# Kernel tuning notes

Measured on AMD Instinct MI355X. Metric: run time of the kernel, lower is better.

Reference implementation:

```python
import jax, jax.numpy as jnp
import numpy as np
import math

B, T, D = 2, 2048, 512      # batch, n_tp, input_dim
DM, H = 64, 16              # per-head d_model, nhead


def setup_inputs() -> dict:
    key = jax.random.key(0)
    ks = jax.random.split(key, 12)
    s = 0.02
    return {
        "data": jax.random.normal(ks[0], (B, T, D), jnp.float32),
        "mask": jax.random.uniform(ks[1], (B, T, D), jnp.float32),
        "wq": jax.random.normal(ks[2], (D, DM * H), jnp.float32) * s,
        "bq": jnp.zeros((DM * H,), jnp.float32),
        "wk": jax.random.normal(ks[3], (D, DM * H), jnp.float32) * s,
        "bk": jnp.zeros((DM * H,), jnp.float32),
        "wv": jax.random.normal(ks[4], (D, DM * H), jnp.float32) * s,
        "bv": jnp.zeros((DM * H,), jnp.float32),
        "wo": jax.random.normal(ks[5], (DM * H, D), jnp.float32) * s,
        "bo": jnp.zeros((D,), jnp.float32),
    }


def reference(data, mask, wq, bq, wk, bk, wv, bv, wo, bo):
    b, t, d = data.shape
    # NOTE: torch code splits proj as (d_model, nhead): head index is fastest-varying
    def split_heads(x):  # [b,t,DM*H] -> [b,H,t,DM]
        return x.reshape(b, t, DM, H).transpose(0, 3, 1, 2)

    q = split_heads(data @ wq + bq)
    k = split_heads(data @ wk + bk)
    v = split_heads(data @ wv + bv)

    scores = jnp.einsum("bhqd,bhkd->bhqk", q, k) / math.sqrt(DM)
    # padded key positions: rows of mask that sum to exactly 0
    pad = (jnp.sum(mask, axis=-1) == 0.0)  # [b, t] (key axis)
    scores = jnp.where(pad[:, None, None, :], -1e9, scores)
    attn = jax.nn.softmax(scores, axis=-1)  # dropout = identity (eval mode)
    out = jnp.einsum("bhqk,bhkd->bhqd", attn, v)
    # merge as (nhead, d_model) — matches torch permute(0,2,1,3).reshape
    out = out.transpose(0, 2, 1, 3).reshape(b, t, H * DM)
    return out @ wo + bo
```

## Files before the change

kernel.cpp:

```cpp
#include <hip/hip_runtime.h>
#include <hip/hip_bf16.h>

#define B_  2
#define T_  2048
#define D_  512
#define DM_ 64
#define H_  16
#define NQ_ (DM_*H_)

typedef __bf16 bf16x8 __attribute__((ext_vector_type(8)));
typedef __bf16 bf16x4 __attribute__((ext_vector_type(4)));
typedef float  f32x4  __attribute__((ext_vector_type(4)));
typedef unsigned int u32;

static __device__ __forceinline__ __bf16 bfc(float x) { return (__bf16)x; }
static __device__ __forceinline__ unsigned short f2bf(float x) {
    __bf16 b = (__bf16)x;
    unsigned short u;
    __builtin_memcpy(&u, &b, 2);
    return u;
}

#if __has_builtin(__builtin_amdgcn_exp2f)
static __device__ __forceinline__ float EXP2(float x) { return __builtin_amdgcn_exp2f(x); }
#else
static __device__ __forceinline__ float EXP2(float x) {
    float r; asm("v_exp_f32 %0, %1\ns_nop 0" : "=v"(r) : "v"(x)); return r;
}
#endif

#define GLOAD16(gp, lp) \
    __builtin_amdgcn_global_load_lds((const __attribute__((address_space(1))) u32*)(gp), \
                                     (__attribute__((address_space(3))) u32*)(lp), 16, 0, 0)

__global__ __launch_bounds__(256)
void prep_kernel(const float* __restrict__ mask, float* __restrict__ padb,
                 const float* __restrict__ data, unsigned short* __restrict__ dataB,
                 const float* __restrict__ wq, const float* __restrict__ wk,
                 const float* __restrict__ wv, unsigned short* __restrict__ btall,
                 const float* __restrict__ wo, unsigned short* __restrict__ wot)
{
    __shared__ float t[32][33];
    const int bid = blockIdx.x;
    const int tid = threadIdx.x;
    if (bid < 1024) {
        const int row  = bid * 4 + (tid >> 6);
        const int lane = tid & 63;
        const float* p = mask + (size_t)row * D_;
        float4 a = *(const float4*)&p[lane * 8];
        float4 b = *(const float4*)&p[lane * 8 + 4];
        float s = a.x + a.y + a.z + a.w + b.x + b.y + b.z + b.w;
#pragma unroll
        for (int off = 32; off; off >>= 1) s += __shfl_down(s, off);
        if (lane == 0) padb[row] = (s == 0.0f) ? -1e9f : 0.0f;
    } else if (bid < 2048) {
        int i = ((bid - 1024) * 256 + tid) * 8;
        float4 a = *(const float4*)&data[i];
        float4 b = *(const float4*)&data[i + 4];
        bf16x8 u = {bfc(a.x), bfc(a.y), bfc(a.z), bfc(a.w),
                    bfc(b.x), bfc(b.y), bfc(b.z), bfc(b.w)};
        *(bf16x8*)&dataB[i] = u;
    } else if (bid < 3584) {
        const int idx = bid - 2048;
        const int z = idx >> 9, rem = idx & 511;
        const int c0 = (rem & 31) * 32, r0 = (rem >> 5) * 32;
        const float* in = (z == 0) ? wq : (z == 1) ? wk : wv;
        unsigned short* out = btall + (size_t)z * NQ_ * D_;
        const int tx = tid & 31, ty = tid >> 5;
#pragma unroll
        for (int i = 0; i < 4; ++i)
            t[ty * 4 + i][tx] = in[(size_t)(r0 + ty * 4 + i) * NQ_ + c0 + tx];
        __syncthreads();
#pragma unroll
        for (int i = 0; i < 4; ++i)
            out[(size_t)(c0 + ty * 4 + i) * D_ + r0 + tx] = f2bf(t[tx][ty * 4 + i]);
    } else {
        const int idx = bid - 3584;
        const int c0 = (idx & 15) * 32, r0 = (idx >> 4) * 32;
        const int tx = tid & 31, ty = tid >> 5;
#pragma unroll
        for (int i = 0; i < 4; ++i)
            t[ty * 4 + i][tx] = wo[(size_t)(r0 + ty * 4 + i) * D_ + c0 + tx];
        __syncthreads();
#pragma unroll
        for (int i = 0; i < 4; ++i)
            wot[(size_t)(c0 + ty * 4 + i) * NQ_ + r0 + tx] = f2bf(t[tx][ty * 4 + i]);
    }
}

__global__ __launch_bounds__(256)
void mgemm_qkv_kernel(const unsigned short* __restrict__ A,
                      const unsigned short* __restrict__ BtAll,
                      const float* __restrict__ bq, const float* __restrict__ bk,
                      const float* __restrict__ bv,
                      unsigned short* __restrict__ Qh, unsigned short* __restrict__ Kh,
                      unsigned short* __restrict__ Vt, float alpha_q)
{
    const int K = D_;
    __shared__ __align__(16) unsigned short Al[2][128 * 64];
    __shared__ __align__(16) unsigned short Bl[2][128 * 64];

    const int tid = threadIdx.x;
    const int w  = tid >> 6, l = tid & 63;
    const int lo = l & 15,  g = l >> 4;
    const int wri = w >> 1, wci = w & 1;
    const int m0 = blockIdx.y * 128, n0 = blockIdx.x * 128;
    const int lrow = l >> 3;
    const int lslot = (l & 7) ^ lrow;

    f32x4 acc[4][4] = {};
    const int nk = K >> 6;

#pragma unroll
    for (int p = 0; p < 4; ++p) {
        int br = w * 32 + p * 8;
        GLOAD16(A     + (size_t)(m0 + br + lrow) * K + lslot * 8, (char*)Al[0] + br * 128);
        GLOAD16(BtAll + (size_t)(n0 + br + lrow) * K + lslot * 8, (char*)Bl[0] + br * 128);
    }
    __syncthreads();

    for (int t = 0; t < nk; ++t) {
        const int cur = t & 1;
        if (t + 1 < nk) {
            const int k0 = (t + 1) << 6;
#pragma unroll
            for (int p = 0; p < 4; ++p) {
                int br = w * 32 + p * 8;
                GLOAD16(A     + (size_t)(m0 + br + lrow) * K + k0 + lslot * 8,
                        (char*)Al[cur ^ 1] + br * 128);
                GLOAD16(BtAll + (size_t)(n0 + br + lrow) * K + k0 + lslot * 8,
                        (char*)Bl[cur ^ 1] + br * 128);
            }
        }
#pragma unroll
        for (int kk = 0; kk < 2; ++kk) {
            bf16x8 af[4], bfr[4];
#pragma unroll
            for (int i = 0; i < 4; ++i) {
                int row = wri * 64 + i * 16 + lo;
                af[i] = *(const bf16x8*)&Al[cur][row * 64 + ((((kk << 2) + g) ^ (row & 7)) << 3)];
                int col = wci * 64 + i * 16 + lo;
                bfr[i] = *(const bf16x8*)&Bl[cur][col * 64 + ((((kk << 2) + g) ^ (col & 7)) << 3)];
            }
#pragma unroll
            for (int i = 0; i < 4; ++i)
#pragma unroll
                for (int j = 0; j < 4; ++j)
                    acc[i][j] = __builtin_amdgcn_mfma_f32_16x16x32_bf16(af[i], bfr[j], acc[i][j], 0, 0, 0);
        }
        __syncthreads();
    }

    const int seg = n0 >> 10;
    const int n0l = n0 & 1023;
    const float* bias = (seg == 0) ? bq : (seg == 1) ? bk : bv;
    const float alpha = (seg == 0) ? alpha_q : 1.0f;
    unsigned short* o16 = (seg == 0) ? Qh : (seg == 1) ? Kh : Vt;

    const int mb = m0 + wri * 64 + g * 4;
    float bb[4];
#pragma unroll
    for (int j = 0; j < 4; ++j) bb[j] = bias[n0l + wci * 64 + j * 16 + lo];
    const int head = lo;
    const int dmb  = (n0l >> 4) + wci * 4;
    if (seg < 2) {
#pragma unroll
        for (int i = 0; i < 4; ++i)
#pragma unroll
            for (int jj = 0; jj < 4; ++jj) {
                int m = mb + i * 16 + jj;
                int t = m & (T_ - 1), bidx = m >> 11;
                bf16x4 u = {bfc((acc[i][0][jj] + bb[0]) * alpha),
                            bfc((acc[i][1][jj] + bb[1]) * alpha),
                            bfc((acc[i][2][jj] + bb[2]) * alpha),
                            bfc((acc[i][3][jj] + bb[3]) * alpha)};
                *(bf16x4*)&o16[(((size_t)(bidx * H_ + head)) * T_ + t) * DM_ + dmb] = u;
            }
    } else {
#pragma unroll
        for (int i = 0; i < 4; ++i)
#pragma unroll
            for (int j = 0; j < 4; ++j) {
                int m = mb + i * 16;
                int t = m & (T_ - 1), bidx = m >> 11;
                bf16x4 u = {bfc(acc[i][j][0] + bb[j]), bfc(acc[i][j][1] + bb[j]),
                            bfc(acc[i][j][2] + bb[j]), bfc(acc[i][j][3] + bb[j])};
                *(bf16x4*)&o16[((size_t)(bidx * H_ + head) * DM_ + dmb + j) * T_ + t] = u;
            }
    }
}

__global__ __launch_bounds__(256)
void mgemm_out_kernel(const unsigned short* __restrict__ A,
                      const unsigned short* __restrict__ Bt,
                      const float* __restrict__ bias, float* __restrict__ out,
                      int M, int N, int K)
{
    __shared__ __align__(16) unsigned short Al[2][64 * 64];
    __shared__ __align__(16) unsigned short Bl[2][128 * 64];

    const int tid = threadIdx.x;
    const int w  = tid >> 6, l = tid & 63;
    const int lo = l & 15,  g = l >> 4;
    const int wri = w >> 1, wci = w & 1;
    const int m0 = blockIdx.y * 64, n0 = blockIdx.x * 128;
    const int lrow = l >> 3;
    const int lslot = (l & 7) ^ lrow;

    f32x4 acc[2][4] = {};
    const int nk = K >> 6;

#pragma unroll
    for (int p = 0; p < 2; ++p) {
        int br = w * 16 + p * 8;
        GLOAD16(A + (size_t)(m0 + br + lrow) * K + lslot * 8, (char*)Al[0] + br * 128);
    }
#pragma unroll
    for (int p = 0; p < 4; ++p) {
        int br = w * 32 + p * 8;
        GLOAD16(Bt + (size_t)(n0 + br + lrow) * K + lslot * 8, (char*)Bl[0] + br * 128);
    }
    __syncthreads();

    for (int t = 0; t < nk; ++t) {
        const int cur = t & 1;
        if (t + 1 < nk) {
            const int k0 = (t + 1) << 6;
#pragma unroll
            for (int p = 0; p < 2; ++p) {
                int br = w * 16 + p * 8;
                GLOAD16(A + (size_t)(m0 + br + lrow) * K + k0 + lslot * 8,
                        (char*)Al[cur ^ 1] + br * 128);
            }
#pragma unroll
            for (int p = 0; p < 4; ++p) {
                int br = w * 32 + p * 8;
                GLOAD16(Bt + (size_t)(n0 + br + lrow) * K + k0 + lslot * 8,
                        (char*)Bl[cur ^ 1] + br * 128);
            }
        }
#pragma unroll
        for (int kk = 0; kk < 2; ++kk) {
            bf16x8 af[2], bfr[4];
#pragma unroll
            for (int i = 0; i < 2; ++i) {
                int row = wri * 32 + i * 16 + lo;
                af[i] = *(const bf16x8*)&Al[cur][row * 64 + ((((kk << 2) + g) ^ (row & 7)) << 3)];
            }
#pragma unroll
            for (int j = 0; j < 4; ++j) {
                int col = wci * 64 + j * 16 + lo;
                bfr[j] = *(const bf16x8*)&Bl[cur][col * 64 + ((((kk << 2) + g) ^ (col & 7)) << 3)];
            }
#pragma unroll
            for (int i = 0; i < 2; ++i)
#pragma unroll
                for (int j = 0; j < 4; ++j)
                    acc[i][j] = __builtin_amdgcn_mfma_f32_16x16x32_bf16(af[i], bfr[j], acc[i][j], 0, 0, 0);
        }
        __syncthreads();
    }

    const int mb = m0 + wri * 32 + g * 4;
#pragma unroll
    for (int j = 0; j < 4; ++j) {
        int n = n0 + wci * 64 + j * 16 + lo;
        float bb = bias[n];
#pragma unroll
        for (int i = 0; i < 2; ++i)
#pragma unroll
            for (int jj = 0; jj < 4; ++jj) {
                int m = mb + i * 16 + jj;
                out[(size_t)m * N + n] = acc[i][j][jj] + bb;
            }
    }
}

__global__ __launch_bounds__(512, 4)
void attn_kernel(const unsigned short* __restrict__ Qh,
                 const unsigned short* __restrict__ Kh,
                 const unsigned short* __restrict__ Vt,
                 const float* __restrict__ padb,
                 unsigned short* __restrict__ ctx)
{
    __shared__ __align__(16) unsigned short Ks[2][64 * 64];
    __shared__ __align__(16) unsigned short Vs[2][64 * 64];
    __shared__ __align__(16) unsigned short Ps[8][16 * 64];

    const int tid  = threadIdx.x;
    const int w    = tid >> 6;
    const int l    = tid & 63;
    const int lo16 = l & 15;
    const int g    = l >> 4;
    const int lrow = l >> 3;
    const int lslot = (l & 7) ^ lrow;

    const int f   = blockIdx.x;
    const int s   = f >> 3;
    const int bh  = (f & 7) * 4 + (s >> 4);
    const int q0  = (s & 15) * 128;
    const int bb  = bh >> 4;
    const int hh  = bh & 15;

    bf16x8 qf[2];
    {
        const unsigned short* Qp =
            Qh + ((size_t)bh * T_ + q0 + w * 16 + lo16) * DM_ + g * 8;
        qf[0] = *(const bf16x8*)(Qp);
        qf[1] = *(const bf16x8*)(Qp + 32);
    }

    const unsigned short* Kg0 = Kh + (size_t)bh * T_ * DM_;
    const unsigned short* Vg0 = Vt + (size_t)bh * DM_ * T_;
    const float* pbase = padb + bb * T_;

    GLOAD16(Kg0 + (size_t)(w * 8 + lrow) * DM_ + lslot * 8, (char*)Ks[0] + w * 1024);
    GLOAD16(Vg0 + (size_t)(w * 8 + lrow) * T_ + lslot * 8, (char*)Vs[0] + w * 1024);
    __syncthreads();

    f32x4 oa[4] = {};
    f32x4 ls4 = {};
    char* Pb = (char*)&Ps[w][0];
    const int rswz = (lo16 & 7) << 4;

    for (int it = 0; it < T_ / 64; ++it) {
        const int cur = it & 1;
        const char* Kc = (const char*)Ks[cur];
        const char* Vc = (const char*)Vs[cur];
        if (it + 1 < T_ / 64) {
            const int ktn = (it + 1) * 64;
            GLOAD16(Kg0 + (size_t)(ktn + w * 8 + lrow) * DM_ + lslot * 8,
                    (char*)Ks[cur ^ 1] + w * 1024);
            GLOAD16(Vg0 + (size_t)(w * 8 + lrow) * T_ + ktn + lslot * 8,
                    (char*)Vs[cur ^ 1] + w * 1024);
        }

        f32x4 sa[4];
#pragma unroll
        for (int nt = 0; nt < 4; ++nt)
            sa[nt] = *(const f32x4*)&pbase[it * 64 + nt * 16 + g * 4];
        __builtin_amdgcn_s_setprio(1);
#pragma unroll
        for (int ks = 0; ks < 2; ++ks) {
#pragma unroll
            for (int nt = 0; nt < 4; ++nt) {
                int row = nt * 16 + lo16;
                int off = (row * 128 + ks * 64 + g * 16) ^ ((row & 7) << 4);
                bf16x8 kf = *(const bf16x8*)(Kc + off);
                sa[nt] = __builtin_amdgcn_mfma_f32_16x16x32_bf16(kf, qf[ks], sa[nt], 0, 0, 0);
            }
        }
        __builtin_amdgcn_s_setprio(0);

#pragma unroll
        for (int nt = 0; nt < 4; ++nt) {
            float e0 = EXP2(sa[nt][0]);
            float e1 = EXP2(sa[nt][1]);
            float e2 = EXP2(sa[nt][2]);
            float e3 = EXP2(sa[nt][3]);
            ls4 += (f32x4){e0, e1, e2, e3};
            bf16x4 pv4 = {bfc(e0), bfc(e1), bfc(e2), bfc(e3)};
            int wb = (lo16 * 128 + nt * 32 + g * 8) ^ rswz;
            *(bf16x4*)(Pb + wb) = pv4;
        }

        __builtin_amdgcn_s_setprio(1);
#pragma unroll
        for (int ks = 0; ks < 2; ++ks) {
            int poff = (lo16 * 128 + ks * 64 + g * 16) ^ rswz;
            bf16x8 pf = *(const bf16x8*)(Pb + poff);
#pragma unroll
            for (int nd = 0; nd < 4; ++nd) {
                int row = nd * 16 + lo16;
                int off = (row * 128 + ks * 64 + g * 16) ^ ((row & 7) << 4);
                bf16x8 vf = *(const bf16x8*)(Vc + off);
                oa[nd] = __builtin_amdgcn_mfma_f32_16x16x32_bf16(vf, pf, oa[nd], 0, 0, 0);
            }
        }
        __builtin_amdgcn_s_setprio(0);

        __syncthreads();
    }

    float lt = (ls4[0] + ls4[1]) + (ls4[2] + ls4[3]);
    lt += __shfl_xor(lt, 16);
    lt += __shfl_xor(lt, 32);
    float linv = 1.0f / lt;
    const size_t crow =
        ((size_t)(bb * T_ + q0 + w * 16 + lo16)) * NQ_ + hh * DM_;
#pragma unroll
    for (int nd = 0; nd < 4; ++nd) {
        bf16x4 u = {bfc(oa[nd][0] * linv), bfc(oa[nd][1] * linv),
                    bfc(oa[nd][2] * linv), bfc(oa[nd][3] * linv)};
        *(bf16x4*)&ctx[crow + nd * 16 + g * 4] = u;
    }
}

extern "C" void kernel_launch(void* const* d_in, const int* in_sizes, int n_in,
                              void* d_out, int out_size, void* d_ws, size_t ws_size,
                              hipStream_t stream) {
    const float* data = (const float*)d_in[0];
    const float* mask = (const float*)d_in[1];
    const float* wq   = (const float*)d_in[2];
    const float* bq   = (const float*)d_in[3];
    const float* wk   = (const float*)d_in[4];
    const float* bk   = (const float*)d_in[5];
    const float* wv   = (const float*)d_in[6];
    const float* bv   = (const float*)d_in[7];
    const float* wo   = (const float*)d_in[8];
    const float* bo   = (const float*)d_in[9];
    float* out = (float*)d_out;

    char* ws = (char*)d_ws;
    const size_t MB = 1024 * 1024;
    unsigned short* Qh    = (unsigned short*)(ws);
    unsigned short* Kh    = (unsigned short*)(ws +  8 * MB);
    unsigned short* Vt    = (unsigned short*)(ws + 16 * MB);
    unsigned short* CTX   = (unsigned short*)(ws + 24 * MB);
    unsigned short* dataB = (unsigned short*)(ws + 32 * MB);
    unsigned short* BtAll = (unsigned short*)(ws + 36 * MB);
    unsigned short* wot   = (unsigned short*)(ws + 39 * MB);
    float*          padb  = (float*)         (ws + 40 * MB);

    const int M = B_ * T_;
    const float alpha_q = 0.125f * 1.44269504089f;

    prep_kernel<<<4096, 256, 0, stream>>>(mask, padb, data, dataB,
                                          wq, wk, wv, BtAll, wo, wot);

    mgemm_qkv_kernel<<<dim3(3 * NQ_ / 128, M / 128), 256, 0, stream>>>(
        dataB, BtAll, bq, bk, bv, Qh, Kh, Vt, alpha_q);

    attn_kernel<<<512, 512, 0, stream>>>(Qh, Kh, Vt, padb, CTX);

    mgemm_out_kernel<<<dim3(D_ / 128, M / 64), 256, 0, stream>>>(
        CTX, wot, bo, out, M, D_, NQ_);
}
```

Measured before the change: 105.4 us.

## Software-pipeline attention loop: overlap PV of previous tile with QK of current

Restructures the attention inner loop into a prologue/steady-state/epilogue software pipeline. Each iteration runs the QK MFMAs and exp for tile i while doing the P·V MFMAs for tile i-1. This uses a double-buffered per-wave P scratch and a triple-buffered V tile in LDS. The pad-bias row is staged once into LDS instead of read from global each iteration, and swizzled offsets are precomputed. The aim is to hide exp/LDS latency behind matrix work, at the cost of more LDS (roughly 8KB extra for pbs plus extra V/P buffers) and register pressure, which could reduce occupancy.

```diff
diff --git a/kernel.cpp b/kernel.cpp
--- a/kernel.cpp
+++ b/kernel.cpp
@@ -7,6 +7,7 @@
 #define DM_ 64
 #define H_  16
 #define NQ_ (DM_*H_)
+#define NT_ (T_/64)
 
 typedef __bf16 bf16x8 __attribute__((ext_vector_type(8)));
 typedef __bf16 bf16x4 __attribute__((ext_vector_type(4)));
@@ -284,8 +285,9 @@
                  unsigned short* __restrict__ ctx)
 {
     __shared__ __align__(16) unsigned short Ks[2][64 * 64];
-    __shared__ __align__(16) unsigned short Vs[2][64 * 64];
-    __shared__ __align__(16) unsigned short Ps[8][16 * 64];
+    __shared__ __align__(16) unsigned short Vs[3][64 * 64];
+    __shared__ __align__(16) unsigned short Ps[8][2][16 * 64];
+    __shared__ __align__(16) float pbs[T_];
 
     const int tid  = threadIdx.x;
     const int w    = tid >> 6;
@@ -302,56 +304,70 @@
     const int bb  = bh >> 4;
     const int hh  = bh & 15;
 
-    bf16x8 qf[2];
+    bf16x8 qf0, qf1;
     {
         const unsigned short* Qp =
             Qh + ((size_t)bh * T_ + q0 + w * 16 + lo16) * DM_ + g * 8;
-        qf[0] = *(const bf16x8*)(Qp);
-        qf[1] = *(const bf16x8*)(Qp + 32);
-    }
-
-    const unsigned short* Kg0 = Kh + (size_t)bh * T_ * DM_;
-    const unsigned short* Vg0 = Vt + (size_t)bh * DM_ * T_;
-    const float* pbase = padb + bb * T_;
-
-    GLOAD16(Kg0 + (size_t)(w * 8 + lrow) * DM_ + lslot * 8, (char*)Ks[0] + w * 1024);
-    GLOAD16(Vg0 + (size_t)(w * 8 + lrow) * T_ + lslot * 8, (char*)Vs[0] + w * 1024);
+        qf0 = *(const bf16x8*)(Qp);
+        qf1 = *(const bf16x8*)(Qp + 32);
+    }
+
+    const unsigned short* kgp =
+        Kh + (size_t)bh * T_ * DM_ + (size_t)(w * 8 + lrow) * DM_ + lslot * 8;
+    const unsigned short* vgp =
+        Vt + (size_t)bh * DM_ * T_ + (size_t)(w * 8 + lrow) * T_ + lslot * 8;
+
+    *(float4*)&pbs[tid * 4] = *(const float4*)(padb + bb * T_ + tid * 4);
+
+    GLOAD16(kgp, (char*)Ks[0] + w * 1024);
+    GLOAD16(vgp, (char*)Vs[0] + w * 1024);
+    kgp += 64 * DM_;
+    vgp += 64;
+
+    const int swz  = (lo16 & 7) << 4;
+    const int off0 = (lo16 * 128 + g * 16) ^ swz;
+    const int off1 = (lo16 * 128 + 64 + g * 16) ^ swz;
+    int pwoff[4];
+#pragma unroll
+    for (int nt = 0; nt < 4; ++nt)
+        pwoff[nt] = (lo16 * 128 + nt * 32 + g * 8) ^ swz;
+
     __syncthreads();
 
     f32x4 oa[4] = {};
     f32x4 ls4 = {};
-    char* Pb = (char*)&Ps[w][0];
-    const int rswz = (lo16 & 7) << 4;
-
-    for (int it = 0; it < T_ / 64; ++it) {
-        const int cur = it & 1;
-        const char* Kc = (const char*)Ks[cur];
-        const char* Vc = (const char*)Vs[cur];
-        if (it + 1 < T_ / 64) {
-            const int ktn = (it + 1) * 64;
-            GLOAD16(Kg0 + (size_t)(ktn + w * 8 + lrow) * DM_ + lslot * 8,
-                    (char*)Ks[cur ^ 1] + w * 1024);
-            GLOAD16(Vg0 + (size_t)(w * 8 + lrow) * T_ + ktn + lslot * 8,
-                    (char*)Vs[cur ^ 1] + w * 1024);
-        }
+    const float* pbp = pbs;
+
+    char* Kc = (char*)Ks[0];
+    char* Kw = (char*)Ks[1];
+    char* Vr = (char*)Vs[2];
+    char* Vn = (char*)Vs[0];
+    char* Vw = (char*)Vs[1];
+    char* Pc = (char*)&Ps[w][0][0];
+    char* Pp = (char*)&Ps[w][1][0];
+
+    {
+        GLOAD16(kgp, Kw + w * 1024);
+        GLOAD16(vgp, Vw + w * 1024);
+        kgp += 64 * DM_;
+        vgp += 64;
 
         f32x4 sa[4];
 #pragma unroll
         for (int nt = 0; nt < 4; ++nt)
-            sa[nt] = *(const f32x4*)&pbase[it * 64 + nt * 16 + g * 4];
+            sa[nt] = *(const f32x4*)&pbp[nt * 16 + g * 4];
         __builtin_amdgcn_s_setprio(1);
 #pragma unroll
-        for (int ks = 0; ks < 2; ++ks) {
-#pragma unroll
-            for (int nt = 0; nt < 4; ++nt) {
-                int row = nt * 16 + lo16;
-                int off = (row * 128 + ks * 64 + g * 16) ^ ((row & 7) << 4);
-                bf16x8 kf = *(const bf16x8*)(Kc + off);
-                sa[nt] = __builtin_amdgcn_mfma_f32_16x16x32_bf16(kf, qf[ks], sa[nt], 0, 0, 0);
-            }
+        for (int nt = 0; nt < 4; ++nt) {
+            bf16x8 kf = *(const bf16x8*)(Kc + off0 + nt * 2048);
+            sa[nt] = __builtin_amdgcn_mfma_f32_16x16x32_bf16(kf, qf0, sa[nt], 0, 0, 0);
+        }
+#pragma unroll
+        for (int nt = 0; nt < 4; ++nt) {
+            bf16x8 kf = *(const bf16x8*)(Kc + off1 + nt * 2048);
+            sa[nt] = __builtin_amdgcn_mfma_f32_16x16x32_bf16(kf, qf1, sa[nt], 0, 0, 0);
         }
         __builtin_amdgcn_s_setprio(0);
-
 #pragma unroll
         for (int nt = 0; nt < 4; ++nt) {
             float e0 = EXP2(sa[nt][0]);
@@ -359,27 +375,90 @@
             float e2 = EXP2(sa[nt][2]);
             float e3 = EXP2(sa[nt][3]);
             ls4 += (f32x4){e0, e1, e2, e3};
-            bf16x4 pv4 = {bfc(e0), bfc(e1), bfc(e2), bfc(e3)};
-            int wb = (lo16 * 128 + nt * 32 + g * 8) ^ rswz;
-            *(bf16x4*)(Pb + wb) = pv4;
-        }
-
+            bf16x4 p4 = {bfc(e0), bfc(e1), bfc(e2), bfc(e3)};
+            *(bf16x4*)(Pc + pwoff[nt]) = p4;
+        }
+        pbp += 64;
+        __syncthreads();
+        char* t0 = Kc; Kc = Kw; Kw = t0;
+        char* tv = Vr; Vr = Vn; Vn = Vw; Vw = tv;
+        char* tp = Pc; Pc = Pp; Pp = tp;
+    }
+
+    for (int it = 1; it < NT_; ++it) {
+        if (it + 1 < NT_) {
+            GLOAD16(kgp, Kw + w * 1024);
+            GLOAD16(vgp, Vw + w * 1024);
+            kgp += 64 * DM_;
+            vgp += 64;
+        }
+
+        f32x4 sa[4];
+#pragma unroll
+        for (int nt = 0; nt < 4; ++nt)
+            sa[nt] = *(const f32x4*)&pbp[nt * 16 + g * 4];
         __builtin_amdgcn_s_setprio(1);
 #pragma unroll
-        for (int ks = 0; ks < 2; ++ks) {
-            int poff = (lo16 * 128 + ks * 64 + g * 16) ^ rswz;
-            bf16x8 pf = *(const bf16x8*)(Pb + poff);
-#pragma unroll
-            for (int nd = 0; nd < 4; ++nd) {
-                int row = nd * 16 + lo16;
-                int off = (row * 128 + ks * 64 + g * 16) ^ ((row & 7) << 4);
-                bf16x8 vf = *(const bf16x8*)(Vc + off);
-                oa[nd] = __builtin_amdgcn_mfma_f32_16x16x32_bf16(vf, pf, oa[nd], 0, 0, 0);
-            }
+        for (int nt = 0; nt < 4; ++nt) {
+            bf16x8 kf = *(const bf16x8*)(Kc + off0 + nt * 2048);
+            sa[nt] = __builtin_amdgcn_mfma_f32_16x16x32_bf16(kf, qf0, sa[nt], 0, 0, 0);
+        }
+#pragma unroll
+        for (int nt = 0; nt < 4; ++nt) {
+            bf16x8 kf = *(const bf16x8*)(Kc + off1 + nt * 2048);
+            sa[nt] = __builtin_amdgcn_mfma_f32_16x16x32_bf16(kf, qf1, sa[nt], 0, 0, 0);
         }
         __builtin_amdgcn_s_setprio(0);
 
+        bf16x8 pf0 = *(const bf16x8*)(Pp + off0);
+        bf16x8 pf1 = *(const bf16x8*)(Pp + off1);
+        bf16x8 vf0[4], vf1[4];
+#pragma unroll
+        for (int nd = 0; nd < 4; ++nd) {
+            vf0[nd] = *(const bf16x8*)(Vr + off0 + nd * 2048);
+            vf1[nd] = *(const bf16x8*)(Vr + off1 + nd * 2048);
+        }
+
+#pragma unroll
+        for (int nt = 0; nt < 4; ++nt) {
+            float e0 = EXP2(sa[nt][0]);
+            float e1 = EXP2(sa[nt][1]);
+            float e2 = EXP2(sa[nt][2]);
+            float e3 = EXP2(sa[nt][3]);
+            ls4 += (f32x4){e0, e1, e2, e3};
+            bf16x4 p4 = {bfc(e0), bfc(e1), bfc(e2), bfc(e3)};
+            *(bf16x4*)(Pc + pwoff[nt]) = p4;
+        }
+
+        __builtin_amdgcn_s_setprio(1);
+#pragma unroll
+        for (int nd = 0; nd < 4; ++nd)
+            oa[nd] = __builtin_amdgcn_mfma_f32_16x16x32_bf16(vf0[nd], pf0, oa[nd], 0, 0, 0);
+#pragma unroll
+        for (int nd = 0; nd < 4; ++nd)
+            oa[nd] = __builtin_amdgcn_mfma_f32_16x16x32_bf16(vf1[nd], pf1, oa[nd], 0, 0, 0);
+        __builtin_amdgcn_s_setprio(0);
+
+        pbp += 64;
         __syncthreads();
+        char* t0 = Kc; Kc = Kw; Kw = t0;
+        char* tv = Vr; Vr = Vn; Vn = Vw; Vw = tv;
+        char* tp = Pc; Pc = Pp; Pp = tp;
+    }
+
+    {
+        bf16x8 pf0 = *(const bf16x8*)(Pp + off0);
+        bf16x8 pf1 = *(const bf16x8*)(Pp + off1);
+#pragma unroll
+        for (int nd = 0; nd < 4; ++nd) {
+            bf16x8 vf = *(const bf16x8*)(Vr + off0 + nd * 2048);
+            oa[nd] = __builtin_amdgcn_mfma_f32_16x16x32_bf16(vf, pf0, oa[nd], 0, 0, 0);
+        }
+#pragma unroll
+        for (int nd = 0; nd < 4; ++nd) {
+            bf16x8 vf = *(const bf16x8*)(Vr + off1 + nd * 2048);
+            oa[nd] = __builtin_amdgcn_mfma_f32_16x16x32_bf16(vf, pf1, oa[nd], 0, 0, 0);
+        }
     }
 
     float lt = (ls4[0] + ls4[1]) + (ls4[2] + ls4[3]);
```

Result: no change. 104.2 us (-1.1%).

## Restructure attention to 32x32 MFMA with register-resident P and software-pipelined PV

Applied to the files above, without the earlier changes.

The attention kernel now runs 4 waves of 32 query rows each and uses 32x32x16 bf16 MFMAs instead of 16x16x32. The softmax probabilities are passed between lanes with cross-half shuffles rather than a round trip through LDS. PV for one tile is deferred into the next iteration, using a triple-buffered V, so the QK^T and exp of tile i+1 can overlap the PV of tile i. The pad bias is staged once into shared memory. The aim is to cut LDS traffic and sync stalls, at the cost of higher register pressure and lower occupancy per block.

```diff
diff --git a/kernel.cpp b/kernel.cpp
--- a/kernel.cpp
+++ b/kernel.cpp
@@ -7,10 +7,12 @@
 #define DM_ 64
 #define H_  16
 #define NQ_ (DM_*H_)
+#define NT_ (T_/64)
 
 typedef __bf16 bf16x8 __attribute__((ext_vector_type(8)));
 typedef __bf16 bf16x4 __attribute__((ext_vector_type(4)));
 typedef float  f32x4  __attribute__((ext_vector_type(4)));
+typedef float  f32x16 __attribute__((ext_vector_type(16)));
 typedef unsigned int u32;
 
 static __device__ __forceinline__ __bf16 bfc(float x) { return (__bf16)x; }
@@ -19,6 +21,9 @@
     unsigned short u;
     __builtin_memcpy(&u, &b, 2);
     return u;
+}
+static __device__ __forceinline__ u32 pack2bf(float a, float b) {
+    return (u32)f2bf(a) | ((u32)f2bf(b) << 16);
 }
 
 #if __has_builtin(__builtin_amdgcn_exp2f)
@@ -276,7 +281,7 @@
     }
 }
 
-__global__ __launch_bounds__(512, 4)
+__global__ __launch_bounds__(256, 2)
 void attn_kernel(const unsigned short* __restrict__ Qh,
                  const unsigned short* __restrict__ Kh,
                  const unsigned short* __restrict__ Vt,
@@ -284,14 +289,15 @@
                  unsigned short* __restrict__ ctx)
 {
     __shared__ __align__(16) unsigned short Ks[2][64 * 64];
-    __shared__ __align__(16) unsigned short Vs[2][64 * 64];
-    __shared__ __align__(16) unsigned short Ps[8][16 * 64];
+    __shared__ __align__(16) unsigned short Vs[3][64 * 64];
+    __shared__ __align__(16) float pbs[T_];
 
     const int tid  = threadIdx.x;
     const int w    = tid >> 6;
     const int l    = tid & 63;
-    const int lo16 = l & 15;
-    const int g    = l >> 4;
+    const int rowa = l & 31;
+    const int h    = l >> 5;
+    const int h4   = h * 4;
     const int lrow = l >> 3;
     const int lslot = (l & 7) ^ lrow;
 
@@ -302,97 +308,159 @@
     const int bb  = bh >> 4;
     const int hh  = bh & 15;
 
-    bf16x8 qf[2];
+    bf16x8 qf[4];
     {
         const unsigned short* Qp =
-            Qh + ((size_t)bh * T_ + q0 + w * 16 + lo16) * DM_ + g * 8;
-        qf[0] = *(const bf16x8*)(Qp);
-        qf[1] = *(const bf16x8*)(Qp + 32);
-    }
-
-    const unsigned short* Kg0 = Kh + (size_t)bh * T_ * DM_;
-    const unsigned short* Vg0 = Vt + (size_t)bh * DM_ * T_;
-    const float* pbase = padb + bb * T_;
-
-    GLOAD16(Kg0 + (size_t)(w * 8 + lrow) * DM_ + lslot * 8, (char*)Ks[0] + w * 1024);
-    GLOAD16(Vg0 + (size_t)(w * 8 + lrow) * T_ + lslot * 8, (char*)Vs[0] + w * 1024);
+            Qh + ((size_t)bh * T_ + q0 + w * 32 + rowa) * DM_ + h * 8;
+#pragma unroll
+        for (int kq = 0; kq < 4; ++kq) qf[kq] = *(const bf16x8*)(Qp + kq * 16);
+    }
+
+    const unsigned short* kgp =
+        Kh + (size_t)bh * T_ * DM_ + (size_t)(w * 16 + lrow) * DM_ + lslot * 8;
+    const unsigned short* vgp =
+        Vt + (size_t)bh * DM_ * T_ + (size_t)(w * 16 + lrow) * T_ + lslot * 8;
+
+    {
+        const float* src = padb + bb * T_ + tid * 8;
+        *(float4*)&pbs[tid * 8]     = *(const float4*)(src);
+        *(float4*)&pbs[tid * 8 + 4] = *(const float4*)(src + 4);
+    }
+
+    GLOAD16(kgp,            (char*)Ks[0] + w * 2048);
+    GLOAD16(kgp + 8 * DM_,  (char*)Ks[0] + w * 2048 + 1024);
+    GLOAD16(vgp,            (char*)Vs[0] + w * 2048);
+    GLOAD16(vgp + 8 * T_,   (char*)Vs[0] + w * 2048 + 1024);
+    kgp += 64 * DM_;
+    vgp += 64;
+
+    const int kbase = rowa * 128;
+    const int sw = rowa & 7;
+    int e[4];
+#pragma unroll
+    for (int i = 0; i < 4; ++i) e[i] = (((2 * i + h) ^ sw) << 4);
+
     __syncthreads();
 
-    f32x4 oa[4] = {};
-    f32x4 ls4 = {};
-    char* Pb = (char*)&Ps[w][0];
-    const int rswz = (lo16 & 7) << 4;
-
-    for (int it = 0; it < T_ / 64; ++it) {
-        const int cur = it & 1;
-        const char* Kc = (const char*)Ks[cur];
-        const char* Vc = (const char*)Vs[cur];
-        if (it + 1 < T_ / 64) {
-            const int ktn = (it + 1) * 64;
-            GLOAD16(Kg0 + (size_t)(ktn + w * 8 + lrow) * DM_ + lslot * 8,
-                    (char*)Ks[cur ^ 1] + w * 1024);
-            GLOAD16(Vg0 + (size_t)(w * 8 + lrow) * T_ + ktn + lslot * 8,
-                    (char*)Vs[cur ^ 1] + w * 1024);
+    f32x16 oa0 = {}, oa1 = {};
+    float lsum = 0.f;
+    bf16x8 pA[4], pB[4];
+    const float* pbp = pbs;
+
+    char* Kc = (char*)Ks[0];
+    char* Kw = (char*)Ks[1];
+    char* Vr = (char*)Vs[2];
+    char* Vn = (char*)Vs[0];
+    char* Vw = (char*)Vs[1];
+
+#define QK_SM(PW, DO_STAGE, DO_PV, PR)                                        \
+    {                                                                         \
+        if (DO_STAGE) {                                                       \
+            GLOAD16(kgp,           Kw + w * 2048);                            \
+            GLOAD16(kgp + 8 * DM_, Kw + w * 2048 + 1024);                     \
+            GLOAD16(vgp,           Vw + w * 2048);                            \
+            GLOAD16(vgp + 8 * T_,  Vw + w * 2048 + 1024);                     \
+            kgp += 64 * DM_;                                                  \
+            vgp += 64;                                                        \
+        }                                                                     \
+        f32x16 sa0, sa1;                                                      \
+        _Pragma("unroll")                                                     \
+        for (int m = 0; m < 4; ++m) {                                         \
+            f32x4 b0 = *(const f32x4*)(pbp + m * 8 + h4);                     \
+            f32x4 b1 = *(const f32x4*)(pbp + 32 + m * 8 + h4);                \
+            sa0[4*m+0] = b0[0]; sa0[4*m+1] = b0[1];                           \
+            sa0[4*m+2] = b0[2]; sa0[4*m+3] = b0[3];                           \
+            sa1[4*m+0] = b1[0]; sa1[4*m+1] = b1[1];                           \
+            sa1[4*m+2] = b1[2]; sa1[4*m+3] = b1[3];                           \
+        }                                                                     \
+        __builtin_amdgcn_s_setprio(1);                                        \
+        _Pragma("unroll")                                                     \
+        for (int kq = 0; kq < 4; ++kq) {                                      \
+            bf16x8 k0 = *(const bf16x8*)(Kc + kbase + e[kq]);                 \
+            bf16x8 k1 = *(const bf16x8*)(Kc + kbase + 4096 + e[kq]);          \
+            sa0 = __builtin_amdgcn_mfma_f32_32x32x16_bf16(k0, qf[kq], sa0, 0, 0, 0); \
+            sa1 = __builtin_amdgcn_mfma_f32_32x32x16_bf16(k1, qf[kq], sa1, 0, 0, 0); \
+        }                                                                     \
+        __builtin_amdgcn_s_setprio(0);                                        \
+        bf16x8 vf0[4], vf1[4];                                                \
+        if (DO_PV) {                                                          \
+            _Pragma("unroll")                                                 \
+            for (int kc = 0; kc < 4; ++kc) {                                  \
+                vf0[kc] = *(const bf16x8*)(Vr + kbase + e[kc]);               \
+                vf1[kc] = *(const bf16x8*)(Vr + kbase + 4096 + e[kc]);        \
+            }                                                                 \
+        }                                                                     \
+        u32 qlo[8], qhi[8];                                                   \
+        _Pragma("unroll")                                                     \
+        for (int m = 0; m < 4; ++m) {                                         \
+            float e0 = EXP2(sa0[4*m+0]), e1 = EXP2(sa0[4*m+1]);               \
+            float e2 = EXP2(sa0[4*m+2]), e3 = EXP2(sa0[4*m+3]);               \
+            lsum += (e0 + e1) + (e2 + e3);                                    \
+            qlo[m] = pack2bf(e0, e1); qhi[m] = pack2bf(e2, e3);               \
+            float f0 = EXP2(sa1[4*m+0]), f1 = EXP2(sa1[4*m+1]);               \
+            float f2 = EXP2(sa1[4*m+2]), f3 = EXP2(sa1[4*m+3]);               \
+            lsum += (f0 + f1) + (f2 + f3);                                    \
+            qlo[4+m] = pack2bf(f0, f1); qhi[4+m] = pack2bf(f2, f3);           \
+        }                                                                     \
+        _Pragma("unroll")                                                     \
+        for (int kc = 0; kc < 4; ++kc) {                                      \
+            u32 a_lo = h ? qlo[2*kc] : qlo[2*kc+1];                           \
+            u32 a_hi = h ? qhi[2*kc] : qhi[2*kc+1];                           \
+            u32 o_lo = h ? qlo[2*kc+1] : qlo[2*kc];                           \
+            u32 o_hi = h ? qhi[2*kc+1] : qhi[2*kc];                           \
+            u32 r_lo = (u32)__shfl_xor((int)a_lo, 32);                        \
+            u32 r_hi = (u32)__shfl_xor((int)a_hi, 32);                        \
+            uint4 uu;                                                         \
+            uu.x = h ? r_lo : o_lo; uu.y = h ? r_hi : o_hi;                   \
+            uu.z = h ? o_lo : r_lo; uu.w = h ? o_hi : r_hi;                   \
+            PW[kc] = *(bf16x8*)&uu;                                           \
+        }                                                                     \
+        if (DO_PV) {                                                          \
+            __builtin_amdgcn_s_setprio(1);                                    \
+            _Pragma("unroll")                                                 \
+            for (int kc = 0; kc < 4; ++kc) {                                  \
+                oa0 = __builtin_amdgcn_mfma_f32_32x32x16_bf16(vf0[kc], PR[kc], oa0, 0, 0, 0); \
+                oa1 = __builtin_amdgcn_mfma_f32_32x32x16_bf16(vf1[kc], PR[kc], oa1, 0, 0, 0); \
+            }                                                                 \
+            __builtin_amdgcn_s_setprio(0);                                    \
+        }                                                                     \
+        pbp += 64;                                                            \
+        __syncthreads();                                                      \
+        { char* tk = Kc; Kc = Kw; Kw = tk;                                    \
+          char* tv = Vr; Vr = Vn; Vn = Vw; Vw = tv; }                         \
+    }
+
+    QK_SM(pA, true, false, pB)
+
+    for (int it = 1; it < NT_ - 1; it += 2) {
+        QK_SM(pB, true, true, pA)
+        QK_SM(pA, (it + 2 < NT_), true, pB)
+    }
+    QK_SM(pB, false, true, pA)
+
+    {
+#pragma unroll
+        for (int kc = 0; kc < 4; ++kc) {
+            bf16x8 v0 = *(const bf16x8*)(Vr + kbase + e[kc]);
+            bf16x8 v1 = *(const bf16x8*)(Vr + kbase + 4096 + e[kc]);
+            oa0 = __builtin_amdgcn_mfma_f32_32x32x16_bf16(v0, pB[kc], oa0, 0, 0, 0);
+            oa1 = __builtin_amdgcn_mfma_f32_32x32x16_bf16(v1, pB[kc], oa1, 0, 0, 0);
         }
-
-        f32x4 sa[4];
-#pragma unroll
-        for (int nt = 0; nt < 4; ++nt)
-            sa[nt] = *(const f32x4*)&pbase[it * 64 + nt * 16 + g * 4];
-        __builtin_amdgcn_s_setprio(1);
-#pragma unroll
-        for (int ks = 0; ks < 2; ++ks) {
-#pragma unroll
-            for (int nt = 0; nt < 4; ++nt) {
-                int row = nt * 16 + lo16;
-                int off = (row * 128 + ks * 64 + g * 16) ^ ((row & 7) << 4);
-                bf16x8 kf = *(const bf16x8*)(Kc + off);
-                sa[nt] = __builtin_amdgcn_mfma_f32_16x16x32_bf16(kf, qf[ks], sa[nt], 0, 0, 0);
-            }
-        }
-        __builtin_amdgcn_s_setprio(0);
-
-#pragma unroll
-        for (int nt = 0; nt < 4; ++nt) {
-            float e0 = EXP2(sa[nt][0]);
-            float e1 = EXP2(sa[nt][1]);
-            float e2 = EXP2(sa[nt][2]);
-            float e3 = EXP2(sa[nt][3]);
-            ls4 += (f32x4){e0, e1, e2, e3};
-            bf16x4 pv4 = {bfc(e0), bfc(e1), bfc(e2), bfc(e3)};
-            int wb = (lo16 * 128 + nt * 32 + g * 8) ^ rswz;
-            *(bf16x4*)(Pb + wb) = pv4;
-        }
-
-        __builtin_amdgcn_s_setprio(1);
-#pragma unroll
-        for (int ks = 0; ks < 2; ++ks) {
-            int poff = (lo16 * 128 + ks * 64 + g * 16) ^ rswz;
-            bf16x8 pf = *(const bf16x8*)(Pb + poff);
-#pragma unroll
-            for (int nd = 0; nd < 4; ++nd) {
-                int row = nd * 16 + lo16;
-                int off = (row * 128 + ks * 64 + g * 16) ^ ((row & 7) << 4);
-                bf16x8 vf = *(const bf16x8*)(Vc + off);
-                oa[nd] = __builtin_amdgcn_mfma_f32_16x16x32_bf16(vf, pf, oa[nd], 0, 0, 0);
-            }
-        }
-        __builtin_amdgcn_s_setprio(0);
-
-        __syncthreads();
-    }
-
-    float lt = (ls4[0] + ls4[1]) + (ls4[2] + ls4[3]);
-    lt += __shfl_xor(lt, 16);
-    lt += __shfl_xor(lt, 32);
+    }
+#undef QK_SM
+
+    float lt = lsum + __shfl_xor(lsum, 32);
     float linv = 1.0f / lt;
     const size_t crow =
-        ((size_t)(bb * T_ + q0 + w * 16 + lo16)) * NQ_ + hh * DM_;
-#pragma unroll
-    for (int nd = 0; nd < 4; ++nd) {
-        bf16x4 u = {bfc(oa[nd][0] * linv), bfc(oa[nd][1] * linv),
-                    bfc(oa[nd][2] * linv), bfc(oa[nd][3] * linv)};
-        *(bf16x4*)&ctx[crow + nd * 16 + g * 4] = u;
+        ((size_t)(bb * T_ + q0 + w * 32 + rowa)) * NQ_ + hh * DM_;
+#pragma unroll
+    for (int m = 0; m < 4; ++m) {
+        bf16x4 u0 = {bfc(oa0[4*m+0] * linv), bfc(oa0[4*m+1] * linv),
+                     bfc(oa0[4*m+2] * linv), bfc(oa0[4*m+3] * linv)};
+        *(bf16x4*)&ctx[crow + 8 * m + h4] = u0;
+        bf16x4 u1 = {bfc(oa1[4*m+0] * linv), bfc(oa1[4*m+1] * linv),
+                     bfc(oa1[4*m+2] * linv), bfc(oa1[4*m+3] * linv)};
+        *(bf16x4*)&ctx[crow + 32 + 8 * m + h4] = u1;
     }
 }
 
@@ -431,7 +499,7 @@
     mgemm_qkv_kernel<<<dim3(3 * NQ_ / 128, M / 128), 256, 0, stream>>>(
         dataB, BtAll, bq, bk, bv, Qh, Kh, Vt, alpha_q);
 
-    attn_kernel<<<512, 512, 0, stream>>>(Qh, Kh, Vt, padb, CTX);
+    attn_kernel<<<512, 256, 0, stream>>>(Qh, Kh, Vt, padb, CTX);
 
     mgemm_out_kernel<<<dim3(D_ / 128, M / 64), 256, 0, stream>>>(
         CTX, wot, bo, out, M, D_, NQ_);
```

New measurement: 114.0 us. 1.08x slower.
